# Optimization experiments

Measured on AMD Instinct MI355X. Metric: run time of the kernel, lower is better.

Reference implementation:

```python
import jax, jax.numpy as jnp
import numpy as np


def setup_inputs() -> dict:
    key = jax.random.key(0)
    k1, k2 = jax.random.split(key)
    B, T, D = 16, 512, 384
    x = jax.random.normal(k1, (B, T, D), dtype=jnp.float32)
    duration = jax.random.randint(k2, (B, T), 0, 8, dtype=jnp.int64)
    return {"x": x, "duration": duration, "max_length": 4096}


def reference(x, duration, max_length):
    # x: [B, T_phon, D] phoneme-level states; duration: [B, T_phon] ints (frames per phoneme).
    # Equivalent of per-batch repeat_interleave(x[b], duration[b]) then pad to max_length,
    # expressed as a single vectorized gather using cumulative-duration offsets.
    B, T, D = x.shape
    cum = jnp.cumsum(duration, axis=1)                       # [B, T]
    total = cum[:, -1]                                       # [B] true expanded lengths
    frames = jnp.arange(max_length)                          # [L]
    # frame j belongs to phoneme i where cum[i-1] <= j < cum[i]
    idx = jax.vmap(lambda c: jnp.searchsorted(c, frames, side='right'))(cum)  # [B, L]
    idx = jnp.minimum(idx, T - 1)
    mask = (frames[None, :] < total[:, None])                # [B, L]
    out = jnp.take_along_axis(x, idx[:, :, None], axis=1)    # [B, L, D]
    out = out * mask[:, :, None].astype(x.dtype)
    # NOTE: with max_length given, original code sets mel_pos = pad(output, max_length),
    # which (output already being padded 2D tensors) returns the output itself. Replicated.
    mel_pos = out
    return (out, mel_pos)
```

## Files before the change

### kernel.cpp

```cpp
#include <hip/hip_runtime.h>


constexpr int B  = 16;
constexpr int T  = 512;
constexpr int D  = 384;
constexpr int ML = 4096;
constexpr int QPF = D / 4;
constexpr int FPB = 16;
constexpr long long OUT_ELEMS = (long long)B * ML * D;

__global__ void lr_scan_kernel(const int* __restrict__ dur, int* __restrict__ cum) {
    __shared__ int s[T];
    const int b = blockIdx.x;
    const int t = threadIdx.x;
    s[t] = dur[b * T + t];
    __syncthreads();
    #pragma unroll
    for (int off = 1; off < T; off <<= 1) {
        int v = (t >= off) ? s[t - off] : 0;
        __syncthreads();
        s[t] += v;
        __syncthreads();
    }
    cum[b * T + t] = s[t];
}

__global__ __launch_bounds__(256)
void lr_expand_kernel(const float4* __restrict__ x, const int* __restrict__ cum,
                      float4* __restrict__ out) {
    __shared__ int sidx[FPB];
    const int blocksPerB = ML / FPB;
    const int b  = blockIdx.x / blocksPerB;
    const int f0 = (blockIdx.x % blocksPerB) * FPB;
    const int* __restrict__ c = cum + b * T;
    const int t = threadIdx.x;

    if (t < FPB) {
        const int f = f0 + t;
        const int total = c[T - 1];
        if (f >= total) {
            sidx[t] = -1;
        } else {
            int lo = 0, hi = T;
            while (lo < hi) {
                int mid = (lo + hi) >> 1;
                if (c[mid] <= f) lo = mid + 1; else hi = mid;
            }
            sidx[t] = (lo < T - 1) ? lo : (T - 1);
        }
    }
    __syncthreads();

    const float4 zero = make_float4(0.f, 0.f, 0.f, 0.f);
    float4* __restrict__ out0 = out;
    float4* __restrict__ out1 = out + OUT_ELEMS / 4;

    #pragma unroll
    for (int j = t; j < FPB * QPF; j += 256) {
        const int fl  = j / QPF;
        const int q   = j - fl * QPF;
        const int idx = sidx[fl];
        const float4 v = (idx >= 0) ? x[((size_t)(b * T + idx)) * QPF + q] : zero;
        const size_t o = ((size_t)(b * ML + f0 + fl)) * QPF + q;
        out0[o] = v;
        out1[o] = v;
    }
}

extern "C" void kernel_launch(void* const* d_in, const int* in_sizes, int n_in,
                              void* d_out, int out_size, void* d_ws, size_t ws_size,
                              hipStream_t stream) {
    const float* x  = (const float*)d_in[0];
    const int* dur  = (const int*)d_in[1];

    int* cum = (int*)d_ws;

    lr_scan_kernel<<<B, T, 0, stream>>>(dur, cum);
    lr_expand_kernel<<<B * (ML / FPB), 256, 0, stream>>>(
        (const float4*)x, cum, (float4*)d_out);
}
```

Before: 42.46 us.

## Fuse duration scan into expand kernel with wave-shuffle prefix sum

Removes the separate scan kernel: each expand block now recomputes the per-batch cumulative durations in shared memory, using a wave-level shuffle scan over 64 lanes plus a cross-wave fixup, then binary-searches against shared memory. Frames per block go from 16 to 32, halving the block count. This saves one launch and a global round trip for the cumsum, at the cost of every block repeating a 512-element scan and extra barriers before the copy.

New measurement: 34.15 us (median of 2 runs). -19.6%, faster.

```diff
diff --git a/kernel.cpp b/kernel.cpp
--- a/kernel.cpp
+++ b/kernel.cpp
@@ -1,68 +1,77 @@
 #include <hip/hip_runtime.h>
 
 
-constexpr int B  = 16;
-constexpr int T  = 512;
-constexpr int D  = 384;
-constexpr int ML = 4096;
+constexpr int B   = 16;
+constexpr int T   = 512;
+constexpr int D   = 384;
+constexpr int ML  = 4096;
 constexpr int QPF = D / 4;
-constexpr int FPB = 16;
-constexpr long long OUT_ELEMS = (long long)B * ML * D;
+constexpr int FPB = 32;
+constexpr int NBLK = B * (ML / FPB);
+constexpr long long OUT_Q = (long long)B * ML * QPF;
 
-__global__ void lr_scan_kernel(const int* __restrict__ dur, int* __restrict__ cum) {
-    __shared__ int s[T];
-    const int b = blockIdx.x;
-    const int t = threadIdx.x;
-    s[t] = dur[b * T + t];
+typedef float vfloat4 __attribute__((ext_vector_type(4)));
+
+__global__ __launch_bounds__(256)
+void lr_fused_kernel(const vfloat4* __restrict__ x, const int* __restrict__ dur,
+                     vfloat4* __restrict__ out) {
+    __shared__ int cum_s[T];
+    __shared__ int wsum[4];
+    __shared__ int sidx[FPB];
+
+    const int blocksPerB = ML / FPB;
+    const int b    = blockIdx.x / blocksPerB;
+    const int f0   = (blockIdx.x % blocksPerB) * FPB;
+    const int t    = threadIdx.x;
+    const int lane = t & 63;
+    const int wid  = t >> 6;
+
+    const int d0 = dur[b * T + 2 * t];
+    const int d1 = dur[b * T + 2 * t + 1];
+    int s = d0 + d1;
+    #pragma unroll
+    for (int off = 1; off < 64; off <<= 1) {
+        int v = __shfl_up(s, off, 64);
+        if (lane >= off) s += v;
+    }
+    if (lane == 63) wsum[wid] = s;
     __syncthreads();
     #pragma unroll
-    for (int off = 1; off < T; off <<= 1) {
-        int v = (t >= off) ? s[t - off] : 0;
-        __syncthreads();
-        s[t] += v;
-        __syncthreads();
-    }
-    cum[b * T + t] = s[t];
-}
+    for (int w = 0; w < 3; ++w)
+        if (w < wid) s += wsum[w];
+    cum_s[2 * t]     = s - d1;
+    cum_s[2 * t + 1] = s;
+    __syncthreads();
 
-__global__ __launch_bounds__(256)
-void lr_expand_kernel(const float4* __restrict__ x, const int* __restrict__ cum,
-                      float4* __restrict__ out) {
-    __shared__ int sidx[FPB];
-    const int blocksPerB = ML / FPB;
-    const int b  = blockIdx.x / blocksPerB;
-    const int f0 = (blockIdx.x % blocksPerB) * FPB;
-    const int* __restrict__ c = cum + b * T;
-    const int t = threadIdx.x;
+    const int total = cum_s[T - 1];
 
     if (t < FPB) {
         const int f = f0 + t;
-        const int total = c[T - 1];
         if (f >= total) {
             sidx[t] = -1;
         } else {
             int lo = 0, hi = T;
             while (lo < hi) {
                 int mid = (lo + hi) >> 1;
-                if (c[mid] <= f) lo = mid + 1; else hi = mid;
+                if (cum_s[mid] <= f) lo = mid + 1; else hi = mid;
             }
             sidx[t] = (lo < T - 1) ? lo : (T - 1);
         }
     }
     __syncthreads();
 
-    const float4 zero = make_float4(0.f, 0.f, 0.f, 0.f);
-    float4* __restrict__ out0 = out;
-    float4* __restrict__ out1 = out + OUT_ELEMS / 4;
+    const vfloat4 zero = {0.f, 0.f, 0.f, 0.f};
+    vfloat4* __restrict__ out1 = out + OUT_Q;
 
     #pragma unroll
     for (int j = t; j < FPB * QPF; j += 256) {
         const int fl  = j / QPF;
         const int q   = j - fl * QPF;
         const int idx = sidx[fl];
-        const float4 v = (idx >= 0) ? x[((size_t)(b * T + idx)) * QPF + q] : zero;
-        const size_t o = ((size_t)(b * ML + f0 + fl)) * QPF + q;
-        out0[o] = v;
+        vfloat4 v = zero;
+        if (idx >= 0) v = x[(size_t)(b * T + idx) * QPF + q];
+        const size_t o = (size_t)(b * ML + f0 + fl) * QPF + q;
+        out[o]  = v;
         out1[o] = v;
     }
 }
@@ -70,12 +79,9 @@
 extern "C" void kernel_launch(void* const* d_in, const int* in_sizes, int n_in,
                               void* d_out, int out_size, void* d_ws, size_t ws_size,
                               hipStream_t stream) {
-    const float* x  = (const float*)d_in[0];
-    const int* dur  = (const int*)d_in[1];
+    const float* x = (const float*)d_in[0];
+    const int* dur = (const int*)d_in[1];
 
-    int* cum = (int*)d_ws;
-
-    lr_scan_kernel<<<B, T, 0, stream>>>(dur, cum);
-    lr_expand_kernel<<<B * (ML / FPB), 256, 0, stream>>>(
-        (const float4*)x, cum, (float4*)d_out);
+    lr_fused_kernel<<<NBLK, 256, 0, stream>>>(
+        (const vfloat4*)x, dur, (vfloat4*)d_out);
 }
```
